# Kernel tuning notes

Hardware: AMD Instinct MI355X
Metric: run time of the kernel (lower is better)

Reference implementation:

```python
import jax, jax.numpy as jnp
import numpy as np

B, N, E, H = 2, 4096, 512, 8
D = E // H  # head size


def setup_inputs() -> dict:
    key = jax.random.key(0)
    ks = jax.random.split(key, 11)
    s = 1.0 / np.sqrt(E)
    inp = {
        'q': jax.random.normal(ks[0], (B, N, E), jnp.float32),
        'k': jax.random.normal(ks[1], (B, N, E), jnp.float32),
        'v': jax.random.normal(ks[2], (B, N, E), jnp.float32),
        'Wq': jax.random.uniform(ks[3], (E, E), jnp.float32, -s, s),
        'bq': jax.random.uniform(ks[4], (E,), jnp.float32, -s, s),
        'Wk': jax.random.uniform(ks[5], (E, E), jnp.float32, -s, s),
        'bk': jax.random.uniform(ks[6], (E,), jnp.float32, -s, s),
        'Wv': jax.random.uniform(ks[7], (E, E), jnp.float32, -s, s),
        'bv': jax.random.uniform(ks[8], (E,), jnp.float32, -s, s),
        'Wo': jax.random.uniform(ks[9], (E, E), jnp.float32, -s, s),
        'bo': jax.random.uniform(ks[10], (E,), jnp.float32, -s, s),
    }
    return inp


def reference(q, k, v, Wq, bq, Wk, bk, Wv, bv, Wo, bo):
    # Linear projections (torch Linear: x @ W.T + b)
    qp = (q @ Wq.T + bq).reshape(B, N, H, D).transpose(0, 2, 1, 3)  # [B,H,N,D]
    kp = (k @ Wk.T + bk).reshape(B, N, H, D).transpose(0, 2, 1, 3)
    vp = (v @ Wv.T + bv).reshape(B, N, H, D).transpose(0, 2, 1, 3)
    scores = jnp.einsum('bhnd,bhmd->bhnm', qp, kp) / jnp.sqrt(jnp.float32(D))
    attn = jax.nn.softmax(scores, axis=-1)
    out = jnp.einsum('bhnm,bhmd->bhnd', attn, vp)  # [B,H,N,D]
    out = out.transpose(0, 2, 1, 3).reshape(B, N, E)
    return out @ Wo.T + bo
```

## Files before the change

kernel.cpp:

```cpp
#include <hip/hip_runtime.h>
#include <hip/hip_bf16.h>
#include <cstddef>
#include <cstdint>


typedef __bf16 bf16_t;
typedef __bf16 bf16x8 __attribute__((ext_vector_type(8)));
typedef __bf16 bf16x4 __attribute__((ext_vector_type(4)));
typedef float  f32x4  __attribute__((ext_vector_type(4)));

#define MFMA_BF16 __builtin_amdgcn_mfma_f32_16x16x32_bf16

static __device__ __forceinline__ bf16x8 cvt2(const float4& a, const float4& b) {
  return bf16x8{(bf16_t)a.x,(bf16_t)a.y,(bf16_t)a.z,(bf16_t)a.w,
                (bf16_t)b.x,(bf16_t)b.y,(bf16_t)b.z,(bf16_t)b.w};
}

static __device__ __forceinline__ uint32_t pk2(float a, float b) {
  uint32_t r;
  asm("v_cvt_pk_bf16_f32 %0, %1, %2" : "=v"(r) : "v"(a), "v"(b));
  return r;
}

__global__ void __launch_bounds__(256)
cvt_bf16(const float* __restrict__ q, const float* __restrict__ k,
         const float* __restrict__ v, const float* __restrict__ Wq,
         const float* __restrict__ Wk, const float* __restrict__ Wv,
         const float* __restrict__ Wo,
         bf16_t* __restrict__ qb, bf16_t* __restrict__ kb,
         bf16_t* __restrict__ vb, bf16_t* __restrict__ wq,
         bf16_t* __restrict__ wk, bf16_t* __restrict__ wv,
         bf16_t* __restrict__ wo)
{
  const int CQ = 524288;
  const int CW = 32768;
  const int TOT = 3 * CQ + 4 * CW;
  const int STRIDE = 2048 * 256;
  for (int c = blockIdx.x * 256 + threadIdx.x; c < TOT; c += STRIDE) {
    const float* src; bf16_t* dst; int off;
    if (c < 3 * CQ) {
      const int t = c >> 19;
      const int r = c & (CQ - 1);
      src = (t == 0) ? q : (t == 1) ? k : v;
      dst = (t == 0) ? qb : (t == 1) ? kb : vb;
      off = r << 3;
    } else {
      const int c2 = c - 3 * CQ;
      const int t = c2 >> 15;
      const int r = c2 & (CW - 1);
      src = (t == 0) ? Wq : (t == 1) ? Wk : (t == 2) ? Wv : Wo;
      dst = (t == 0) ? wq : (t == 1) ? wk : (t == 2) ? wv : wo;
      off = r << 3;
    }
    const float4 a = *(const float4*)(src + off);
    const float4 b = *(const float4*)(src + off + 4);
    *(bf16x8*)(dst + off) = cvt2(a, b);
  }
}

__global__ void __launch_bounds__(256, 2)
qkv_proj(const bf16_t* __restrict__ qb, const bf16_t* __restrict__ kb,
         const bf16_t* __restrict__ vb,
         const bf16_t* __restrict__ Wqb, const float* __restrict__ bq,
         const bf16_t* __restrict__ Wkb, const float* __restrict__ bk,
         const bf16_t* __restrict__ Wvb, const float* __restrict__ bv,
         bf16_t* __restrict__ Qp, bf16_t* __restrict__ Kp,
         bf16_t* __restrict__ Vt, float qscale)
{
  __shared__ __align__(16) bf16_t As[2][128 * 72];
  __shared__ __align__(16) bf16_t Bs[2][128 * 72];
  const int l     = blockIdx.x;
  const int slice = l >> 8;
  const int inner = l & 255;
  const int mtile = ((inner >> 5) << 3) | (inner & 7);
  const int ntile = (inner >> 3) & 3;
  const int tid   = threadIdx.x;
  const int w     = tid >> 6;
  const int lane  = tid & 63;
  const int lr    = lane & 15;
  const int quad  = lane >> 4;
  const int wm    = w & 1;
  const int wn    = w >> 1;
  const int xrow  = tid >> 1, xcol = (tid & 1) << 5;

  const bf16_t* Xb   = (slice == 0) ? qb  : (slice == 1) ? kb  : vb;
  const bf16_t* W    = (slice == 0) ? Wqb : (slice == 1) ? Wkb : Wvb;
  const float*  bias = (slice == 0) ? bq  : (slice == 1) ? bk  : bv;
  const float scale  = (slice == 0) ? qscale : 1.0f;

  float bvv[4];
#pragma unroll
  for (int ci = 0; ci < 4; ++ci) bvv[ci] = bias[ntile * 128 + wn * 64 + ci * 16 + lr];

  f32x4 acc[4][4] = {};
  bf16x8 xa[4], wa[4];

#pragma unroll
  for (int j = 0; j < 4; ++j) {
    xa[j] = *(const bf16x8*)(Xb + (size_t)(mtile * 128 + xrow) * 512 + xcol + j * 8);
    wa[j] = *(const bf16x8*)(W  + (size_t)(ntile * 128 + xrow) * 512 + xcol + j * 8);
  }
#pragma unroll
  for (int j = 0; j < 4; ++j) {
    *(bf16x8*)(&As[0][xrow * 72 + xcol + j * 8]) = xa[j];
    *(bf16x8*)(&Bs[0][xrow * 72 + xcol + j * 8]) = wa[j];
  }
  __syncthreads();

  for (int it = 0; it < 8; ++it) {
    const int cur = it & 1, nxt = cur ^ 1;
    if (it != 7) {
      const int k0 = (it + 1) << 6;
#pragma unroll
      for (int j = 0; j < 4; ++j) {
        xa[j] = *(const bf16x8*)(Xb + (size_t)(mtile * 128 + xrow) * 512 + k0 + xcol + j * 8);
        wa[j] = *(const bf16x8*)(W  + (size_t)(ntile * 128 + xrow) * 512 + k0 + xcol + j * 8);
      }
    }
    bf16x8 af[4][2], bfr[4][2];
#pragma unroll
    for (int mi = 0; mi < 4; ++mi)
#pragma unroll
      for (int kh = 0; kh < 2; ++kh)
        af[mi][kh] = *(const bf16x8*)(&As[cur][(wm * 64 + mi * 16 + lr) * 72 + (kh * 4 + quad) * 8]);
#pragma unroll
    for (int ci = 0; ci < 4; ++ci)
#pragma unroll
      for (int kh = 0; kh < 2; ++kh)
        bfr[ci][kh] = *(const bf16x8*)(&Bs[cur][(wn * 64 + ci * 16 + lr) * 72 + (kh * 4 + quad) * 8]);
#pragma unroll
    for (int mi = 0; mi < 4; ++mi)
#pragma unroll
      for (int ci = 0; ci < 4; ++ci) {
        acc[mi][ci] = MFMA_BF16(af[mi][0], bfr[ci][0], acc[mi][ci], 0, 0, 0);
        acc[mi][ci] = MFMA_BF16(af[mi][1], bfr[ci][1], acc[mi][ci], 0, 0, 0);
      }
    if (it != 7) {
#pragma unroll
      for (int j = 0; j < 4; ++j) {
        *(bf16x8*)(&As[nxt][xrow * 72 + xcol + j * 8]) = xa[j];
        *(bf16x8*)(&Bs[nxt][xrow * 72 + xcol + j * 8]) = wa[j];
      }
    }
    __syncthreads();
  }

  bf16_t* outQK = (slice == 0) ? Qp : Kp;
#pragma unroll
  for (int mi = 0; mi < 4; ++mi) {
    const int gm0 = mtile * 128 + wm * 64 + mi * 16 + quad * 4;
#pragma unroll
    for (int ci = 0; ci < 4; ++ci) {
      const int gc = ntile * 128 + wn * 64 + ci * 16 + lr;
      const int h = gc >> 6, dd = gc & 63;
      if (slice < 2) {
#pragma unroll
        for (int r = 0; r < 4; ++r) {
          const int gm = gm0 + r;
          const int b = gm >> 12, n = gm & 4095;
          outQK[(size_t)((b * 8 + h) * 4096 + n) * 64 + dd] =
              (bf16_t)((acc[mi][ci][r] + bvv[ci]) * scale);
        }
      } else {
        const int b = gm0 >> 12, n0 = gm0 & 4095;
        bf16x4 pk;
#pragma unroll
        for (int r = 0; r < 4; ++r) pk[r] = (bf16_t)(acc[mi][ci][r] + bvv[ci]);
        *(bf16x4*)(Vt + (size_t)((b * 8 + h) * 64 + dd) * 4096 + n0) = pk;
      }
    }
  }
}

__global__ void __launch_bounds__(256, 2)
o_proj(const bf16_t* __restrict__ Xb, const bf16_t* __restrict__ W,
       const float* __restrict__ bias, float* __restrict__ out)
{
  __shared__ __align__(16) bf16_t As[2][128 * 72];
  __shared__ __align__(16) bf16_t Bs[2][64 * 72];
  const int l     = blockIdx.x;
  const int mtile = ((l >> 6) << 3) | (l & 7);
  const int ntile = (l >> 3) & 7;
  const int tid   = threadIdx.x;
  const int w     = tid >> 6;
  const int lane  = tid & 63;
  const int lr    = lane & 15;
  const int quad  = lane >> 4;
  const int wm    = w & 1;
  const int wn    = w >> 1;
  const int xrow  = tid >> 1, xcol = (tid & 1) << 5;
  const int wrow  = tid >> 2, wcol = (tid & 3) << 4;

  float bvv[2];
#pragma unroll
  for (int ci = 0; ci < 2; ++ci) bvv[ci] = bias[ntile * 64 + wn * 32 + ci * 16 + lr];

  f32x4 acc[4][2] = {};
  bf16x8 xb[4], wb[2];

#pragma unroll
  for (int j = 0; j < 4; ++j)
    xb[j] = *(const bf16x8*)(Xb + (size_t)(mtile * 128 + xrow) * 512 + xcol + j * 8);
#pragma unroll
  for (int j = 0; j < 2; ++j)
    wb[j] = *(const bf16x8*)(W + (size_t)(ntile * 64 + wrow) * 512 + wcol + j * 8);
#pragma unroll
  for (int j = 0; j < 4; ++j)
    *(bf16x8*)(&As[0][xrow * 72 + xcol + j * 8]) = xb[j];
#pragma unroll
  for (int j = 0; j < 2; ++j)
    *(bf16x8*)(&Bs[0][wrow * 72 + wcol + j * 8]) = wb[j];
  __syncthreads();

  for (int it = 0; it < 8; ++it) {
    const int cur = it & 1, nxt = cur ^ 1;
    if (it != 7) {
      const int k0 = (it + 1) << 6;
#pragma unroll
      for (int j = 0; j < 4; ++j)
        xb[j] = *(const bf16x8*)(Xb + (size_t)(mtile * 128 + xrow) * 512 + k0 + xcol + j * 8);
#pragma unroll
      for (int j = 0; j < 2; ++j)
        wb[j] = *(const bf16x8*)(W + (size_t)(ntile * 64 + wrow) * 512 + k0 + wcol + j * 8);
    }
    bf16x8 af[4][2], bfr[2][2];
#pragma unroll
    for (int mi = 0; mi < 4; ++mi)
#pragma unroll
      for (int kh = 0; kh < 2; ++kh)
        af[mi][kh] = *(const bf16x8*)(&As[cur][(wm * 64 + mi * 16 + lr) * 72 + (kh * 4 + quad) * 8]);
#pragma unroll
    for (int ci = 0; ci < 2; ++ci)
#pragma unroll
      for (int kh = 0; kh < 2; ++kh)
        bfr[ci][kh] = *(const bf16x8*)(&Bs[cur][(wn * 32 + ci * 16 + lr) * 72 + (kh * 4 + quad) * 8]);
#pragma unroll
    for (int mi = 0; mi < 4; ++mi)
#pragma unroll
      for (int ci = 0; ci < 2; ++ci) {
        acc[mi][ci] = MFMA_BF16(af[mi][0], bfr[ci][0], acc[mi][ci], 0, 0, 0);
        acc[mi][ci] = MFMA_BF16(af[mi][1], bfr[ci][1], acc[mi][ci], 0, 0, 0);
      }
    if (it != 7) {
#pragma unroll
      for (int j = 0; j < 4; ++j)
        *(bf16x8*)(&As[nxt][xrow * 72 + xcol + j * 8]) = xb[j];
#pragma unroll
      for (int j = 0; j < 2; ++j)
        *(bf16x8*)(&Bs[nxt][wrow * 72 + wcol + j * 8]) = wb[j];
    }
    __syncthreads();
  }

#pragma unroll
  for (int mi = 0; mi < 4; ++mi) {
    const int gm0 = mtile * 128 + wm * 64 + mi * 16 + quad * 4;
#pragma unroll
    for (int ci = 0; ci < 2; ++ci) {
      const int gc = ntile * 64 + wn * 32 + ci * 16 + lr;
#pragma unroll
      for (int r = 0; r < 4; ++r)
        out[(size_t)(gm0 + r) * 512 + gc] = acc[mi][ci][r] + bvv[ci];
    }
  }
}

__global__ void __launch_bounds__(256, 2)
flash_attn(const bf16_t* __restrict__ Qp, const bf16_t* __restrict__ Kp,
           const bf16_t* __restrict__ Vt, bf16_t* __restrict__ Oc)
{
  __shared__ __align__(16) bf16_t Klds[2][64 * 72];
  __shared__ __align__(16) bf16_t Vlds[2][64 * 72];

  const int tid  = threadIdx.x;
  const int w    = tid >> 6;
  const int lane = tid & 63, lr = lane & 15, quad = lane >> 4;
  const int bh   = blockIdx.x;
  const int qt0  = blockIdx.y * 128 + w * 32;

  const bf16_t* Qh = Qp + (size_t)bh * 4096 * 64;
  const bf16_t* Kh = Kp + (size_t)bh * 4096 * 64;
  const bf16_t* Vh = Vt + (size_t)bh * 64 * 4096;

  const int srow = w * 16 + (lane >> 2);
  const int scol = (lane & 3) << 4;

  bf16x8 qf[2][2];
#pragma unroll
  for (int qi = 0; qi < 2; ++qi)
#pragma unroll
    for (int kh = 0; kh < 2; ++kh)
      qf[qi][kh] = *(const bf16x8*)(Qh + (size_t)(qt0 + qi * 16 + lr) * 64 + kh * 32 + quad * 8);

  bf16x8 kst[2], vst[2];
#pragma unroll
  for (int j = 0; j < 2; ++j) {
    kst[j] = *(const bf16x8*)(Kh + (size_t)srow * 64 + scol + j * 8);
    vst[j] = *(const bf16x8*)(Vh + (size_t)srow * 4096 + scol + j * 8);
  }
#pragma unroll
  for (int j = 0; j < 2; ++j) {
    *(bf16x8*)(&Klds[0][srow * 72 + scol + j * 8]) = kst[j];
    *(bf16x8*)(&Vlds[0][srow * 72 + scol + j * 8]) = vst[j];
  }
  __syncthreads();

  f32x4 acc[2][4] = {};
  float lsum[2] = {0.f, 0.f};
  const f32x4 zero = {0.f, 0.f, 0.f, 0.f};

  for (int it = 0; it < 64; ++it) {
    const int cur = it & 1, nxt = cur ^ 1;

    if (it != 63) {
      const int kvn = (it + 1) << 6;
#pragma unroll
      for (int j = 0; j < 2; ++j) {
        kst[j] = *(const bf16x8*)(Kh + (size_t)(kvn + srow) * 64 + scol + j * 8);
        vst[j] = *(const bf16x8*)(Vh + (size_t)srow * 4096 + kvn + scol + j * 8);
      }
    }

    bf16x8 kf[4][2];
#pragma unroll
    for (int mt = 0; mt < 4; ++mt)
#pragma unroll
      for (int kh = 0; kh < 2; ++kh)
        kf[mt][kh] = *(const bf16x8*)(&Klds[cur][(mt * 16 + lr) * 72 + (kh * 4 + quad) * 8]);
    bf16x8 vf[4][2];
#pragma unroll
    for (int t = 0; t < 4; ++t)
#pragma unroll
      for (int kvh = 0; kvh < 2; ++kvh)
        vf[t][kvh] = *(const bf16x8*)(&Vlds[cur][(t * 16 + lr) * 72 + (kvh * 4 + quad) * 8]);

    f32x4 sT[4][2];
#pragma unroll
    for (int mt = 0; mt < 4; ++mt)
#pragma unroll
      for (int qi = 0; qi < 2; ++qi) {
        sT[mt][qi] = MFMA_BF16(kf[mt][0], qf[qi][0], zero, 0, 0, 0);
        sT[mt][qi] = MFMA_BF16(kf[mt][1], qf[qi][1], sT[mt][qi], 0, 0, 0);
      }

    bf16x8 pa[2][2];
#pragma unroll
    for (int qi = 0; qi < 2; ++qi) {
      uint32_t ap[4], bp[4];
#pragma unroll
      for (int mt = 0; mt < 4; ++mt) {
        float p0 = __builtin_amdgcn_exp2f(sT[mt][qi][0]);
        float p1 = __builtin_amdgcn_exp2f(sT[mt][qi][1]);
        float p2 = __builtin_amdgcn_exp2f(sT[mt][qi][2]);
        float p3 = __builtin_amdgcn_exp2f(sT[mt][qi][3]);
        lsum[qi] += (p0 + p1) + (p2 + p3);
        ap[mt] = pk2(p0, p1);
        bp[mt] = pk2(p2, p3);
      }
#pragma unroll
      for (int kvh = 0; kvh < 2; ++kvh) {
        uint32_t xa_ = ap[2 * kvh], ya_ = ap[2 * kvh + 1];
        asm("v_permlane32_swap_b32 %0, %1" : "+v"(xa_), "+v"(ya_));
        asm("v_permlane16_swap_b32 %0, %1" : "+v"(xa_), "+v"(ya_));
        uint32_t xb_ = bp[2 * kvh], yb_ = bp[2 * kvh + 1];
        asm("v_permlane32_swap_b32 %0, %1" : "+v"(xb_), "+v"(yb_));
        asm("v_permlane16_swap_b32 %0, %1" : "+v"(xb_), "+v"(yb_));
        union { uint32_t u[4]; bf16x8 v; } pu;
        pu.u[0] = xa_; pu.u[1] = xb_; pu.u[2] = ya_; pu.u[3] = yb_;
        pa[qi][kvh] = pu.v;
      }
    }

#pragma unroll
    for (int t = 0; t < 4; ++t)
#pragma unroll
      for (int qi = 0; qi < 2; ++qi) {
        acc[qi][t] = MFMA_BF16(pa[qi][0], vf[t][0], acc[qi][t], 0, 0, 0);
        acc[qi][t] = MFMA_BF16(pa[qi][1], vf[t][1], acc[qi][t], 0, 0, 0);
      }

    if (it != 63) {
#pragma unroll
      for (int j = 0; j < 2; ++j) {
        *(bf16x8*)(&Klds[nxt][srow * 72 + scol + j * 8]) = kst[j];
        *(bf16x8*)(&Vlds[nxt][srow * 72 + scol + j * 8]) = vst[j];
      }
    }
    __syncthreads();
  }

#pragma unroll
  for (int qi = 0; qi < 2; ++qi) {
    lsum[qi] += __shfl_xor(lsum[qi], 16);
    lsum[qi] += __shfl_xor(lsum[qi], 32);
  }

  const int b = bh >> 3, h = bh & 7;
  bf16_t* Ob = Oc + (size_t)b * 4096 * 512 + h * 64;
#pragma unroll
  for (int qi = 0; qi < 2; ++qi) {
    float inv[4];
#pragma unroll
    for (int r = 0; r < 4; ++r)
      inv[r] = 1.0f / __shfl(lsum[qi], quad * 4 + r);
#pragma unroll
    for (int t = 0; t < 4; ++t)
#pragma unroll
      for (int r = 0; r < 4; ++r) {
        const int n = qt0 + qi * 16 + quad * 4 + r;
        Ob[(size_t)n * 512 + t * 16 + lr] = (bf16_t)(acc[qi][t][r] * inv[r]);
      }
  }
}

extern "C" void kernel_launch(void* const* d_in, const int* in_sizes, int n_in,
                              void* d_out, int out_size, void* d_ws, size_t ws_size,
                              hipStream_t stream)
{
  const float* q  = (const float*)d_in[0];
  const float* k  = (const float*)d_in[1];
  const float* v  = (const float*)d_in[2];
  const float* Wq = (const float*)d_in[3];
  const float* bq = (const float*)d_in[4];
  const float* Wk = (const float*)d_in[5];
  const float* bk = (const float*)d_in[6];
  const float* Wv = (const float*)d_in[7];
  const float* bv = (const float*)d_in[8];
  const float* Wo = (const float*)d_in[9];
  const float* bo = (const float*)d_in[10];

  const size_t HEAD_ELEMS = (size_t)2 * 8 * 4096 * 64;
  const size_t W_ELEMS    = (size_t)512 * 512;

  bf16_t* base = (bf16_t*)d_ws;
  bf16_t* qb  = base;
  bf16_t* kb  = qb + HEAD_ELEMS;
  bf16_t* vb  = kb + HEAD_ELEMS;
  bf16_t* Qp  = vb + HEAD_ELEMS;
  bf16_t* Kp  = Qp + HEAD_ELEMS;
  bf16_t* Vt  = Kp + HEAD_ELEMS;
  bf16_t* wqb = Vt + HEAD_ELEMS;
  bf16_t* wkb = wqb + W_ELEMS;
  bf16_t* wvb = wkb + W_ELEMS;
  bf16_t* wob = wvb + W_ELEMS;
  bf16_t* Oc  = qb;

  const float qscale = 0.125f * 1.44269504f;

  cvt_bf16<<<dim3(2048), 256, 0, stream>>>(q, k, v, Wq, Wk, Wv, Wo,
                                           qb, kb, vb, wqb, wkb, wvb, wob);
  qkv_proj<<<dim3(768), 256, 0, stream>>>(qb, kb, vb, wqb, bq, wkb, bk,
                                          wvb, bv, Qp, Kp, Vt, qscale);
  flash_attn<<<dim3(16, 32), 256, 0, stream>>>(Qp, Kp, Vt, Oc);
  o_proj<<<dim3(512), 256, 0, stream>>>(Oc, wob, bo, (float*)d_out);
}
```

Before: 225.0 us.

## Single-buffer GEMM LDS, stage QKV epilogue through LDS, shrink o_proj tiles

qkv_proj drops from double-buffered to single-buffered LDS, adding an extra barrier per k-step, and raises launch bounds to 3 blocks per CU. Its epilogue now stages the bias-added bf16 tile through LDS (transposed for V) so global writes become coalesced 16-byte stores instead of scattered 2-byte or 8-byte stores. o_proj moves to 64x64 tiles with single-buffered LDS, 1024 blocks and 4 blocks per CU, trading per-block reuse for more parallelism and occupancy. The extra barriers cut the load/compute overlap inside each block.

```diff
diff --git a/kernel.cpp b/kernel.cpp
--- a/kernel.cpp
+++ b/kernel.cpp
@@ -58,7 +58,7 @@
   }
 }
 
-__global__ void __launch_bounds__(256, 2)
+__global__ void __launch_bounds__(256, 3)
 qkv_proj(const bf16_t* __restrict__ qb, const bf16_t* __restrict__ kb,
          const bf16_t* __restrict__ vb,
          const bf16_t* __restrict__ Wqb, const float* __restrict__ bq,
@@ -67,8 +67,10 @@
          bf16_t* __restrict__ Qp, bf16_t* __restrict__ Kp,
          bf16_t* __restrict__ Vt, float qscale)
 {
-  __shared__ __align__(16) bf16_t As[2][128 * 72];
-  __shared__ __align__(16) bf16_t Bs[2][128 * 72];
+  __shared__ __align__(16) bf16_t S[2 * 128 * 72];
+  bf16_t* As = S;
+  bf16_t* Bs = S + 128 * 72;
+
   const int l     = blockIdx.x;
   const int slice = l >> 8;
   const int inner = l & 255;
@@ -102,13 +104,12 @@
   }
 #pragma unroll
   for (int j = 0; j < 4; ++j) {
-    *(bf16x8*)(&As[0][xrow * 72 + xcol + j * 8]) = xa[j];
-    *(bf16x8*)(&Bs[0][xrow * 72 + xcol + j * 8]) = wa[j];
+    *(bf16x8*)(&As[xrow * 72 + xcol + j * 8]) = xa[j];
+    *(bf16x8*)(&Bs[xrow * 72 + xcol + j * 8]) = wa[j];
   }
   __syncthreads();
 
   for (int it = 0; it < 8; ++it) {
-    const int cur = it & 1, nxt = cur ^ 1;
     if (it != 7) {
       const int k0 = (it + 1) << 6;
 #pragma unroll
@@ -122,12 +123,12 @@
     for (int mi = 0; mi < 4; ++mi)
 #pragma unroll
       for (int kh = 0; kh < 2; ++kh)
-        af[mi][kh] = *(const bf16x8*)(&As[cur][(wm * 64 + mi * 16 + lr) * 72 + (kh * 4 + quad) * 8]);
+        af[mi][kh] = *(const bf16x8*)(&As[(wm * 64 + mi * 16 + lr) * 72 + (kh * 4 + quad) * 8]);
 #pragma unroll
     for (int ci = 0; ci < 4; ++ci)
 #pragma unroll
       for (int kh = 0; kh < 2; ++kh)
-        bfr[ci][kh] = *(const bf16x8*)(&Bs[cur][(wn * 64 + ci * 16 + lr) * 72 + (kh * 4 + quad) * 8]);
+        bfr[ci][kh] = *(const bf16x8*)(&Bs[(wn * 64 + ci * 16 + lr) * 72 + (kh * 4 + quad) * 8]);
 #pragma unroll
     for (int mi = 0; mi < 4; ++mi)
 #pragma unroll
@@ -135,52 +136,69 @@
         acc[mi][ci] = MFMA_BF16(af[mi][0], bfr[ci][0], acc[mi][ci], 0, 0, 0);
         acc[mi][ci] = MFMA_BF16(af[mi][1], bfr[ci][1], acc[mi][ci], 0, 0, 0);
       }
+    __syncthreads();
     if (it != 7) {
 #pragma unroll
       for (int j = 0; j < 4; ++j) {
-        *(bf16x8*)(&As[nxt][xrow * 72 + xcol + j * 8]) = xa[j];
-        *(bf16x8*)(&Bs[nxt][xrow * 72 + xcol + j * 8]) = wa[j];
-      }
-    }
+        *(bf16x8*)(&As[xrow * 72 + xcol + j * 8]) = xa[j];
+        *(bf16x8*)(&Bs[xrow * 72 + xcol + j * 8]) = wa[j];
+      }
+      __syncthreads();
+    }
+  }
+
+  bf16_t (*Ct)[136] = (bf16_t (*)[136])S;
+  if (slice < 2) {
+    bf16_t* outQK = (slice == 0) ? Qp : Kp;
+#pragma unroll
+    for (int mi = 0; mi < 4; ++mi)
+#pragma unroll
+      for (int ci = 0; ci < 4; ++ci)
+#pragma unroll
+        for (int r = 0; r < 4; ++r)
+          Ct[wm * 64 + mi * 16 + quad * 4 + r][wn * 64 + ci * 16 + lr] =
+              (bf16_t)((acc[mi][ci][r] + bvv[ci]) * scale);
     __syncthreads();
-  }
-
-  bf16_t* outQK = (slice == 0) ? Qp : Kp;
-#pragma unroll
-  for (int mi = 0; mi < 4; ++mi) {
-    const int gm0 = mtile * 128 + wm * 64 + mi * 16 + quad * 4;
-#pragma unroll
-    for (int ci = 0; ci < 4; ++ci) {
-      const int gc = ntile * 128 + wn * 64 + ci * 16 + lr;
-      const int h = gc >> 6, dd = gc & 63;
-      if (slice < 2) {
-#pragma unroll
-        for (int r = 0; r < 4; ++r) {
-          const int gm = gm0 + r;
-          const int b = gm >> 12, n = gm & 4095;
-          outQK[(size_t)((b * 8 + h) * 4096 + n) * 64 + dd] =
-              (bf16_t)((acc[mi][ci][r] + bvv[ci]) * scale);
-        }
-      } else {
-        const int b = gm0 >> 12, n0 = gm0 & 4095;
-        bf16x4 pk;
-#pragma unroll
-        for (int r = 0; r < 4; ++r) pk[r] = (bf16_t)(acc[mi][ci][r] + bvv[ci]);
-        *(bf16x4*)(Vt + (size_t)((b * 8 + h) * 64 + dd) * 4096 + n0) = pk;
-      }
-    }
-  }
-}
-
-__global__ void __launch_bounds__(256, 2)
+    const int r2 = tid >> 1, half = tid & 1;
+    const int gm = mtile * 128 + r2;
+    const int b = gm >> 12, n = gm & 4095;
+    const int gc0 = ntile * 128 + half * 64;
+    const int h = gc0 >> 6;
+    bf16_t* dst = outQK + (size_t)((b * 8 + h) * 4096 + n) * 64;
+#pragma unroll
+    for (int j = 0; j < 8; ++j)
+      *(bf16x8*)(dst + j * 8) = *(const bf16x8*)(&Ct[r2][half * 64 + j * 8]);
+  } else {
+#pragma unroll
+    for (int mi = 0; mi < 4; ++mi)
+#pragma unroll
+      for (int ci = 0; ci < 4; ++ci)
+#pragma unroll
+        for (int r = 0; r < 4; ++r)
+          Ct[wn * 64 + ci * 16 + lr][wm * 64 + mi * 16 + quad * 4 + r] =
+              (bf16_t)(acc[mi][ci][r] + bvv[ci]);
+    __syncthreads();
+    const int dline = tid >> 1, half = tid & 1;
+    const int gc = ntile * 128 + dline;
+    const int h = gc >> 6, dd = gc & 63;
+    const int b = (mtile * 128) >> 12;
+    const int n0 = (mtile * 128) & 4095;
+    bf16_t* dst = Vt + (size_t)((b * 8 + h) * 64 + dd) * 4096 + n0 + half * 64;
+#pragma unroll
+    for (int j = 0; j < 8; ++j)
+      *(bf16x8*)(dst + j * 8) = *(const bf16x8*)(&Ct[dline][half * 64 + j * 8]);
+  }
+}
+
+__global__ void __launch_bounds__(256, 4)
 o_proj(const bf16_t* __restrict__ Xb, const bf16_t* __restrict__ W,
        const float* __restrict__ bias, float* __restrict__ out)
 {
-  __shared__ __align__(16) bf16_t As[2][128 * 72];
-  __shared__ __align__(16) bf16_t Bs[2][64 * 72];
+  __shared__ __align__(16) bf16_t As[64 * 72];
+  __shared__ __align__(16) bf16_t Bs[64 * 72];
   const int l     = blockIdx.x;
-  const int mtile = ((l >> 6) << 3) | (l & 7);
-  const int ntile = (l >> 3) & 7;
+  const int mtile = l >> 3;
+  const int ntile = l & 7;
   const int tid   = threadIdx.x;
   const int w     = tid >> 6;
   const int lane  = tid & 63;
@@ -188,73 +206,68 @@
   const int quad  = lane >> 4;
   const int wm    = w & 1;
   const int wn    = w >> 1;
-  const int xrow  = tid >> 1, xcol = (tid & 1) << 5;
-  const int wrow  = tid >> 2, wcol = (tid & 3) << 4;
+  const int xrow  = tid >> 2, xcol = (tid & 3) << 4;
 
   float bvv[2];
 #pragma unroll
   for (int ci = 0; ci < 2; ++ci) bvv[ci] = bias[ntile * 64 + wn * 32 + ci * 16 + lr];
 
-  f32x4 acc[4][2] = {};
-  bf16x8 xb[4], wb[2];
-
-#pragma unroll
-  for (int j = 0; j < 4; ++j)
-    xb[j] = *(const bf16x8*)(Xb + (size_t)(mtile * 128 + xrow) * 512 + xcol + j * 8);
-#pragma unroll
-  for (int j = 0; j < 2; ++j)
-    wb[j] = *(const bf16x8*)(W + (size_t)(ntile * 64 + wrow) * 512 + wcol + j * 8);
-#pragma unroll
-  for (int j = 0; j < 4; ++j)
-    *(bf16x8*)(&As[0][xrow * 72 + xcol + j * 8]) = xb[j];
-#pragma unroll
-  for (int j = 0; j < 2; ++j)
-    *(bf16x8*)(&Bs[0][wrow * 72 + wcol + j * 8]) = wb[j];
+  f32x4 acc[2][2] = {};
+  bf16x8 xb[2], wb[2];
+
+#pragma unroll
+  for (int j = 0; j < 2; ++j) {
+    xb[j] = *(const bf16x8*)(Xb + (size_t)(mtile * 64 + xrow) * 512 + xcol + j * 8);
+    wb[j] = *(const bf16x8*)(W  + (size_t)(ntile * 64 + xrow) * 512 + xcol + j * 8);
+  }
+#pragma unroll
+  for (int j = 0; j < 2; ++j) {
+    *(bf16x8*)(&As[xrow * 72 + xcol + j * 8]) = xb[j];
+    *(bf16x8*)(&Bs[xrow * 72 + xcol + j * 8]) = wb[j];
+  }
   __syncthreads();
 
   for (int it = 0; it < 8; ++it) {
-    const int cur = it & 1, nxt = cur ^ 1;
     if (it != 7) {
       const int k0 = (it + 1) << 6;
 #pragma unroll
-      for (int j = 0; j < 4; ++j)
-        xb[j] = *(const bf16x8*)(Xb + (size_t)(mtile * 128 + xrow) * 512 + k0 + xcol + j * 8);
-#pragma unroll
-      for (int j = 0; j < 2; ++j)
-        wb[j] = *(const bf16x8*)(W + (size_t)(ntile * 64 + wrow) * 512 + k0 + wcol + j * 8);
-    }
-    bf16x8 af[4][2], bfr[2][2];
-#pragma unroll
-    for (int mi = 0; mi < 4; ++mi)
+      for (int j = 0; j < 2; ++j) {
+        xb[j] = *(const bf16x8*)(Xb + (size_t)(mtile * 64 + xrow) * 512 + k0 + xcol + j * 8);
+        wb[j] = *(const bf16x8*)(W  + (size_t)(ntile * 64 + xrow) * 512 + k0 + xcol + j * 8);
+      }
+    }
+    bf16x8 af[2][2], bfr[2][2];
+#pragma unroll
+    for (int mi = 0; mi < 2; ++mi)
 #pragma unroll
       for (int kh = 0; kh < 2; ++kh)
-        af[mi][kh] = *(const bf16x8*)(&As[cur][(wm * 64 + mi * 16 + lr) * 72 + (kh * 4 + quad) * 8]);
+        af[mi][kh] = *(const bf16x8*)(&As[(wm * 32 + mi * 16 + lr) * 72 + (kh * 4 + quad) * 8]);
 #pragma unroll
     for (int ci = 0; ci < 2; ++ci)
 #pragma unroll
       for (int kh = 0; kh < 2; ++kh)
-        bfr[ci][kh] = *(const bf16x8*)(&Bs[cur][(wn * 32 + ci * 16 + lr) * 72 + (kh * 4 + quad) * 8]);
-#pragma unroll
-    for (int mi = 0; mi < 4; ++mi)
+        bfr[ci][kh] = *(const bf16x8*)(&Bs[(wn * 32 + ci * 16 + lr) * 72 + (kh * 4 + quad) * 8]);
+#pragma unroll
+    for (int mi = 0; mi < 2; ++mi)
 #pragma unroll
       for (int ci = 0; ci < 2; ++ci) {
         acc[mi][ci] = MFMA_BF16(af[mi][0], bfr[ci][0], acc[mi][ci], 0, 0, 0);
         acc[mi][ci] = MFMA_BF16(af[mi][1], bfr[ci][1], acc[mi][ci], 0, 0, 0);
       }
+    __syncthreads();
     if (it != 7) {
 #pragma unroll
-      for (int j = 0; j < 4; ++j)
-        *(bf16x8*)(&As[nxt][xrow * 72 + xcol + j * 8]) = xb[j];
-#pragma unroll
-      for (int j = 0; j < 2; ++j)
-        *(bf16x8*)(&Bs[nxt][wrow * 72 + wcol + j * 8]) = wb[j];
-    }
-    __syncthreads();
-  }
-
-#pragma unroll
-  for (int mi = 0; mi < 4; ++mi) {
-    const int gm0 = mtile * 128 + wm * 64 + mi * 16 + quad * 4;
+      for (int j = 0; j < 2; ++j) {
+        *(bf16x8*)(&As[xrow * 72 + xcol + j * 8]) = xb[j];
+        *(bf16x8*)(&Bs[xrow * 72 + xcol + j * 8]) = wb[j];
+      }
+      __syncthreads();
+    }
+  }
+
+#pragma unroll
+  for (int mi = 0; mi < 2; ++mi) {
+    const int gm0 = mtile * 64 + wm * 32 + mi * 16 + quad * 4;
 #pragma unroll
     for (int ci = 0; ci < 2; ++ci) {
       const int gc = ntile * 64 + wn * 32 + ci * 16 + lr;
@@ -452,5 +465,5 @@
   qkv_proj<<<dim3(768), 256, 0, stream>>>(qb, kb, vb, wqb, bq, wkb, bk,
                                           wvb, bv, Qp, Kp, Vt, qscale);
   flash_attn<<<dim3(16, 32), 256, 0, stream>>>(Qp, Kp, Vt, Oc);
-  o_proj<<<dim3(512), 256, 0, stream>>>(Oc, wob, bo, (float*)d_out);
-}
+  o_proj<<<dim3(1024), 256, 0, stream>>>(Oc, wob, bo, (float*)d_out);
+}
```

Result: no change. 226.7 us (+0.8%).
